# Kernel tuning notes

Hardware: AMD Instinct MI355X
Metric: run time of the kernel (lower is better)

The kernel has to match this reference:

```python
import jax, jax.numpy as jnp
import numpy as np

DIM = 2048
HEADS = 16
B = 2
T = 2048


def setup_inputs() -> dict:
    key = jax.random.key(0)
    k_x, k_qkv, k_out, k_b = jax.random.split(key, 4)
    inv = DIM ** -0.5
    return {
        "x": jax.random.normal(k_x, (B, T, DIM), dtype=jnp.float32),
        "w_qkv": jax.random.normal(k_qkv, (DIM, 3 * DIM), dtype=jnp.float32) * inv,
        "w_out": jax.random.normal(k_out, (DIM, DIM), dtype=jnp.float32) * inv,
        "b_out": jnp.zeros((DIM,), dtype=jnp.float32),
    }


def reference(x, w_qkv, w_out, b_out):
    b, t, e = x.shape
    h = HEADS
    d = e // h
    scale = d ** -0.5
    qkv = x @ w_qkv                              # [b, t, 3e]
    q, k, v = jnp.split(qkv, 3, axis=-1)
    # [b, t, e] -> [b, h, t, d]
    q, k, v = (a.reshape(b, t, h, d).transpose(0, 2, 1, 3) for a in (q, k, v))
    dots = jnp.einsum("bhid,bhjd->bhij", q, k) * scale  # [b, h, t, t]
    causal_mask = jnp.triu(jnp.ones((t, t), dtype=bool), k=1)  # True where j > i
    dots = jnp.where(causal_mask[None, None, :, :], -jnp.inf, dots)
    attn = jax.nn.softmax(dots, axis=-1)
    out = jnp.einsum("bhij,bhjd->bhid", attn, v)  # [b, h, t, d]
    out = out.transpose(0, 2, 1, 3).reshape(b, t, e)
    return out @ w_out + b_out
```

## Files before the change

### kernel.cpp

```cpp
#include <hip/hip_runtime.h>
#include <stdint.h>

#define BATCH 2
#define TDIM 2048
#define EDIM 2048
#define NH 16
#define HD 128
#define E3 6144
#define MROWS 4096

typedef short v8bf __attribute__((ext_vector_type(8)));
typedef float v4f  __attribute__((ext_vector_type(4)));

typedef __attribute__((address_space(3))) uint8_t lds_u8;
typedef __attribute__((address_space(1))) uint8_t glb_u8;

__device__ __forceinline__ void gload16(const void* g, void* l) {
    __builtin_amdgcn_global_load_lds((const glb_u8*)g, (lds_u8*)l, 16, 0, 0);
}

__device__ __forceinline__ ushort f2bf(float f) {
    uint32_t u = __float_as_uint(f);
    return (ushort)((u + 0x7fffu + ((u >> 16) & 1u)) >> 16);
}

__global__ void cvtx_kernel(const float* __restrict__ in, ushort* __restrict__ out, int n) {
    int i = (blockIdx.x * 256 + threadIdx.x) * 4;
    const int stride = gridDim.x * 256 * 4;
    for (; i < n; i += stride) {
        const float4 v = *reinterpret_cast<const float4*>(in + i);
        ushort4 o = make_ushort4(f2bf(v.x), f2bf(v.y), f2bf(v.z), f2bf(v.w));
        *reinterpret_cast<ushort4*>(out + i) = o;
    }
}

__global__ void tcvt_kernel(const float* __restrict__ in, ushort* __restrict__ out, int R, int C) {
    __shared__ float t[32][33];
    const int tc = blockIdx.x * 32;
    const int tr = blockIdx.y * 32;
    const int tid = threadIdx.x;
    const int row = tid >> 3, c4 = (tid & 7) * 4;
    const float4 v = *reinterpret_cast<const float4*>(in + (size_t)(tr + row) * C + tc + c4);
    t[row][c4] = v.x; t[row][c4 + 1] = v.y; t[row][c4 + 2] = v.z; t[row][c4 + 3] = v.w;
    __syncthreads();
    const int oc = tid >> 3, r4 = (tid & 7) * 4;
    ushort4 o = make_ushort4(f2bf(t[r4][oc]), f2bf(t[r4 + 1][oc]),
                             f2bf(t[r4 + 2][oc]), f2bf(t[r4 + 3][oc]));
    *reinterpret_cast<ushort4*>(out + (size_t)(tc + oc) * R + tr + r4) = o;
}

__global__ void vtrans_kernel(const ushort* __restrict__ qkv, ushort* __restrict__ vt) {
    __shared__ ushort t[32][33];
    const int bh = blockIdx.z;
    const int b = bh >> 4, h = bh & 15;
    const int tr = blockIdx.x * 32;
    const int tc = blockIdx.y * 32;
    const int tid = threadIdx.x;
    const int row = tid >> 3, c4 = (tid & 7) * 4;
    const ushort4 v = *reinterpret_cast<const ushort4*>(
        qkv + (size_t)(b * TDIM + tr + row) * E3 + 2 * EDIM + h * HD + tc + c4);
    t[row][c4] = v.x; t[row][c4 + 1] = v.y; t[row][c4 + 2] = v.z; t[row][c4 + 3] = v.w;
    __syncthreads();
    const int oc = tid >> 3, r4 = (tid & 7) * 4;
    ushort4 o = make_ushort4(t[r4][oc], t[r4 + 1][oc], t[r4 + 2][oc], t[r4 + 3][oc]);
    *reinterpret_cast<ushort4*>(vt + (size_t)(bh * HD + tc + oc) * TDIM + tr + r4) = o;
}

template <int OUTF32>
__global__ void gemm_kernel(const ushort* __restrict__ A, const ushort* __restrict__ Bt,
                            void* __restrict__ Cv, const float* __restrict__ bias,
                            int Mdim, int Ndim, int Kdim) {
    __shared__ __align__(16) ushort As[128 * 64];
    __shared__ __align__(16) ushort Bs[128 * 64];
    const int tid = threadIdx.x;
    const int lane = tid & 63;
    const int wv = tid >> 6;
    const int l4 = lane >> 4, l16 = lane & 15;
    const int nbn = Ndim >> 7;
    const int nwg = (Mdim >> 7) * nbn;
    int bid = blockIdx.x;
    bid = (bid & 7) * (nwg >> 3) + (bid >> 3);
    const int bm = bid / nbn, bn = bid % nbn;
    const int wr = wv >> 1, wc = wv & 1;

    const ushort* Abase = A + (size_t)(bm * 128) * Kdim;
    const ushort* Bbase = Bt + (size_t)(bn * 128) * Kdim;

    v4f acc[4][4] = {};

    for (int k0 = 0; k0 < Kdim; k0 += 64) {
#pragma unroll
        for (int i = 0; i < 4; ++i) {
            const int c = i * 256 + tid;
            const int row = c >> 3;
            const int kc = (c & 7) ^ (row & 7);
            gload16(Abase + (size_t)row * Kdim + k0 + kc * 8, &As[(i * 256 + wv * 64) * 8]);
        }
#pragma unroll
        for (int i = 0; i < 4; ++i) {
            const int c = i * 256 + tid;
            const int row = c >> 3;
            const int kc = (c & 7) ^ (row & 7);
            gload16(Bbase + (size_t)row * Kdim + k0 + kc * 8, &Bs[(i * 256 + wv * 64) * 8]);
        }
        __syncthreads();
#pragma unroll
        for (int kk = 0; kk < 2; ++kk) {
            v8bf af[4], bfr[4];
#pragma unroll
            for (int m = 0; m < 4; ++m) {
                const int r = wr * 64 + m * 16 + l16;
                const int slot = (kk * 4 + l4) ^ (r & 7);
                af[m] = *reinterpret_cast<const v8bf*>(&As[r * 64 + slot * 8]);
            }
#pragma unroll
            for (int n = 0; n < 4; ++n) {
                const int r = wc * 64 + n * 16 + l16;
                const int slot = (kk * 4 + l4) ^ (r & 7);
                bfr[n] = *reinterpret_cast<const v8bf*>(&Bs[r * 64 + slot * 8]);
            }
#pragma unroll
            for (int m = 0; m < 4; ++m)
#pragma unroll
                for (int n = 0; n < 4; ++n)
                    acc[m][n] = __builtin_amdgcn_mfma_f32_16x16x32_bf16(af[m], bfr[n], acc[m][n], 0, 0, 0);
        }
        __syncthreads();
    }

    const int r0 = bm * 128 + wr * 64 + l4 * 4;
    const int c0 = bn * 128 + wc * 64 + l16;
    if (OUTF32) {
        float* C = (float*)Cv;
#pragma unroll
        for (int n = 0; n < 4; ++n) {
            const float bv = bias[c0 + n * 16];
#pragma unroll
            for (int m = 0; m < 4; ++m)
#pragma unroll
                for (int j = 0; j < 4; ++j)
                    C[(size_t)(r0 + m * 16 + j) * Ndim + c0 + n * 16] = acc[m][n][j] + bv;
        }
    } else {
        ushort* C = (ushort*)Cv;
#pragma unroll
        for (int n = 0; n < 4; ++n)
#pragma unroll
            for (int m = 0; m < 4; ++m)
#pragma unroll
                for (int j = 0; j < 4; ++j)
                    C[(size_t)(r0 + m * 16 + j) * Ndim + c0 + n * 16] = f2bf(acc[m][n][j]);
    }
}

__global__ __launch_bounds__(256, 2) void flash_kernel(const ushort* __restrict__ qkv,
                                                       const ushort* __restrict__ vt,
                                                       ushort* __restrict__ ao) {
    __shared__ __align__(16) ushort Kl[2][64 * 128];
    __shared__ __align__(16) ushort Vl[2][128 * 64];
    __shared__ __align__(16) ushort Pl[128 * 64];

    const int xi = blockIdx.x;
    const int ti = (xi & 1) ? (xi >> 1) : (15 - (xi >> 1));
    const int h = blockIdx.y;
    const int b = blockIdx.z;
    const int tid = threadIdx.x;
    const int lane = tid & 63;
    const int wv = tid >> 6;
    const int l4 = lane >> 4, l16 = lane & 15;

    const int rbs[2]  = {ti * 64 + wv * 16, TDIM - 64 * (ti + 1) + wv * 16};
    const int diag[2] = {ti, 31 - ti};
    const int nkt = 32 - ti;

    v8bf qf[2][4];
#pragma unroll
    for (int mg = 0; mg < 2; ++mg) {
        const ushort* qp = qkv + (size_t)(b * TDIM + rbs[mg] + l16) * E3 + h * HD + l4 * 8;
#pragma unroll
        for (int d0 = 0; d0 < 4; ++d0) {
            v8bf r = *reinterpret_cast<const v8bf*>(qp + d0 * 32);
            v8bf o;
#pragma unroll
            for (int e = 0; e < 8; ++e) {
                const float f = __uint_as_float(((uint32_t)(ushort)r[e]) << 16) * 0.08838834764831845f;
                o[e] = (short)f2bf(f);
            }
            qf[mg][d0] = o;
        }
    }

    float mrun[2][4], lrun[2][4];
#pragma unroll
    for (int mg = 0; mg < 2; ++mg)
#pragma unroll
        for (int j = 0; j < 4; ++j) { mrun[mg][j] = -1e30f; lrun[mg][j] = 0.0f; }
    v4f oacc[2][8] = {};

    const ushort* kbase = qkv + (size_t)(b * TDIM) * E3 + EDIM + h * HD;
    const ushort* vbase = vt + (size_t)((b * 16 + h) * HD) * TDIM;

#define STAGE(BUF, KT)                                                                        \
    do {                                                                                      \
        _Pragma("unroll") for (int i = 0; i < 4; ++i) {                                       \
            const int c = i * 256 + tid;                                                      \
            const int row = c >> 4;                                                           \
            const int dc = (c & 15) ^ (row & 7);                                              \
            gload16(kbase + (size_t)((KT) * 64 + row) * E3 + dc * 8,                          \
                    &Kl[BUF][(i * 256 + wv * 64) * 8]);                                       \
        }                                                                                     \
        _Pragma("unroll") for (int i = 0; i < 4; ++i) {                                       \
            const int c = i * 256 + tid;                                                      \
            const int row = c >> 3;                                                           \
            const int jc = (c & 7) ^ (row & 7);                                               \
            gload16(vbase + (size_t)row * TDIM + (KT) * 64 + jc * 8,                          \
                    &Vl[BUF][(i * 256 + wv * 64) * 8]);                                       \
        }                                                                                     \
    } while (0)

    STAGE(0, 0);
    __syncthreads();
    int cur = 0;

    for (int kt = 0; kt < nkt; ++kt) {
        if (kt + 1 < nkt) STAGE(cur ^ 1, kt + 1);

        const bool act0 = (kt <= diag[0]);
        const ushort* Kb = &Kl[cur][0];
        const ushort* Vb = &Vl[cur][0];

        v4f s[2][4] = {};
#pragma unroll
        for (int d0 = 0; d0 < 4; ++d0) {
            v8bf kf[4];
#pragma unroll
            for (int kvn = 0; kvn < 4; ++kvn) {
                const int r = kvn * 16 + l16;
                const int slot = (d0 * 4 + l4) ^ (r & 7);
                kf[kvn] = *reinterpret_cast<const v8bf*>(&Kb[r * 128 + slot * 8]);
            }
#pragma unroll
            for (int kvn = 0; kvn < 4; ++kvn) {
                if (act0)
                    s[0][kvn] = __builtin_amdgcn_mfma_f32_16x16x32_bf16(qf[0][d0], kf[kvn], s[0][kvn], 0, 0, 0);
                s[1][kvn] = __builtin_amdgcn_mfma_f32_16x16x32_bf16(qf[1][d0], kf[kvn], s[1][kvn], 0, 0, 0);
            }
        }

#pragma unroll
        for (int mg = 0; mg < 2; ++mg) {
            if (mg == 0 && !act0) continue;

            float sv[4][4];
#pragma unroll
            for (int kvn = 0; kvn < 4; ++kvn)
#pragma unroll
                for (int j = 0; j < 4; ++j)
                    sv[kvn][j] = s[mg][kvn][j];

            if (kt == diag[mg]) {
                const int rg = rbs[mg] + l4 * 4;
#pragma unroll
                for (int kvn = 0; kvn < 4; ++kvn) {
                    const int cg = kt * 64 + kvn * 16 + l16;
#pragma unroll
                    for (int j = 0; j < 4; ++j)
                        if (cg > rg + j) sv[kvn][j] = -__builtin_inff();
                }
            }

            float pm[4], dmax = -1e30f;
#pragma unroll
            for (int j = 0; j < 4; ++j) {
                float m0 = fmaxf(fmaxf(sv[0][j], sv[1][j]), fmaxf(sv[2][j], sv[3][j]));
                m0 = fmaxf(m0, __shfl_xor(m0, 1));
                m0 = fmaxf(m0, __shfl_xor(m0, 2));
                m0 = fmaxf(m0, __shfl_xor(m0, 4));
                m0 = fmaxf(m0, __shfl_xor(m0, 8));
                pm[j] = m0;
                dmax = fmaxf(dmax, m0 - mrun[mg][j]);
            }
            if (!__all(dmax <= 8.0f)) {
                float corr[4];
#pragma unroll
                for (int j = 0; j < 4; ++j) {
                    const float mn = fmaxf(mrun[mg][j], pm[j]);
                    corr[j] = __expf(mrun[mg][j] - mn);
                    mrun[mg][j] = mn;
                    lrun[mg][j] *= corr[j];
                }
#pragma unroll
                for (int n = 0; n < 8; ++n)
#pragma unroll
                    for (int j = 0; j < 4; ++j)
                        oacc[mg][n][j] *= corr[j];
            }

            float p[4][4];
#pragma unroll
            for (int kvn = 0; kvn < 4; ++kvn)
#pragma unroll
                for (int j = 0; j < 4; ++j)
                    p[kvn][j] = __expf(sv[kvn][j] - mrun[mg][j]);
#pragma unroll
            for (int j = 0; j < 4; ++j)
                lrun[mg][j] += p[0][j] + p[1][j] + p[2][j] + p[3][j];

            const int row = wv * 32 + mg * 16 + l4 * 4;
#pragma unroll
            for (int kvn = 0; kvn < 4; ++kvn) {
                const int cc = kvn * 2 + (l16 >> 3);
#pragma unroll
                for (int j = 0; j < 4; ++j) {
                    const int r = row + j;
                    Pl[r * 64 + ((cc ^ (r & 7)) * 8) + (l16 & 7)] = f2bf(p[kvn][j]);
                }
            }
        }

#pragma unroll
        for (int kk = 0; kk < 2; ++kk) {
            v8bf pf[2];
#pragma unroll
            for (int mg = 0; mg < 2; ++mg) {
                if (mg == 0 && !act0) continue;
                const int r = wv * 32 + mg * 16 + l16;
                const int slot = (kk * 4 + l4) ^ (r & 7);
                pf[mg] = *reinterpret_cast<const v8bf*>(&Pl[r * 64 + slot * 8]);
            }
#pragma unroll
            for (int n = 0; n < 8; ++n) {
                const int dr = n * 16 + l16;
                const int slot = (kk * 4 + l4) ^ (dr & 7);
                v8bf vf = *reinterpret_cast<const v8bf*>(&Vb[dr * 64 + slot * 8]);
                if (act0)
                    oacc[0][n] = __builtin_amdgcn_mfma_f32_16x16x32_bf16(pf[0], vf, oacc[0][n], 0, 0, 0);
                oacc[1][n] = __builtin_amdgcn_mfma_f32_16x16x32_bf16(pf[1], vf, oacc[1][n], 0, 0, 0);
            }
        }
        __syncthreads();
        cur ^= 1;
    }
#undef STAGE

#pragma unroll
    for (int mg = 0; mg < 2; ++mg) {
        float inv[4];
#pragma unroll
        for (int j = 0; j < 4; ++j) {
            float l = lrun[mg][j];
            l += __shfl_xor(l, 1);
            l += __shfl_xor(l, 2);
            l += __shfl_xor(l, 4);
            l += __shfl_xor(l, 8);
            inv[j] = 1.0f / l;
        }
        ushort* aop = ao + (size_t)(b * TDIM + rbs[mg] + l4 * 4) * EDIM + h * HD + l16;
#pragma unroll
        for (int n = 0; n < 8; ++n)
#pragma unroll
            for (int j = 0; j < 4; ++j)
                aop[(size_t)j * EDIM + n * 16] = f2bf(oacc[mg][n][j] * inv[j]);
    }
}

extern "C" void kernel_launch(void* const* d_in, const int* in_sizes, int n_in,
                              void* d_out, int out_size, void* d_ws, size_t ws_size,
                              hipStream_t stream) {
    (void)in_sizes; (void)n_in; (void)out_size; (void)ws_size;
    const float* x     = (const float*)d_in[0];
    const float* w_qkv = (const float*)d_in[1];
    const float* w_out = (const float*)d_in[2];
    const float* b_out = (const float*)d_in[3];

    uint8_t* ws = (uint8_t*)d_ws;
    ushort* qkv   = (ushort*)(ws);
    ushort* woutT = (ushort*)(ws + 50331648u);
    ushort* xb    = (ushort*)(ws + 58720256u);
    ushort* wqkvT = (ushort*)(ws + 75497472u);
    ushort* vtb   = xb;
    ushort* ao    = wqkvT;

    cvtx_kernel<<<2048, 256, 0, stream>>>(x, xb, MROWS * EDIM);
    tcvt_kernel<<<dim3(E3 / 32, EDIM / 32), 256, 0, stream>>>(w_qkv, wqkvT, EDIM, E3);
    tcvt_kernel<<<dim3(EDIM / 32, EDIM / 32), 256, 0, stream>>>(w_out, woutT, EDIM, EDIM);

    gemm_kernel<0><<<(MROWS / 128) * (E3 / 128), 256, 0, stream>>>(
        xb, wqkvT, (void*)qkv, nullptr, MROWS, E3, EDIM);

    vtrans_kernel<<<dim3(TDIM / 32, HD / 32, BATCH * NH), 256, 0, stream>>>(qkv, vtb);

    flash_kernel<<<dim3(16, NH, BATCH), 256, 0, stream>>>(qkv, vtb, ao);

    gemm_kernel<1><<<(MROWS / 128) * (EDIM / 128), 256, 0, stream>>>(
        ao, woutT, d_out, b_out, MROWS, EDIM, EDIM);
}
```

Before: 265.1 us.

## Add 256x256 double-buffered QKV GEMM kernel with 8 waves

Replaces the 128x128 QKV projection GEMM with a new 256x256-tile kernel using 512 threads, double-buffered LDS staging via global_load_lds, and a two-stage prefetch pipeline with explicit waitcnt and barriers. Larger tiles raise arithmetic intensity and cut global and L2 traffic, and the prefetch overlaps loads with MFMA work. The kernel uses 128 KB of LDS and many accumulator registers per thread, which limits occupancy, and the grid shrinks to 384 workgroups, which may balance poorly across CUs. Local variable renames in the old GEMM are cosmetic.

```diff
diff --git a/kernel.cpp b/kernel.cpp
--- a/kernel.cpp
+++ b/kernel.cpp
@@ -64,6 +64,120 @@
     const int oc = tid >> 3, r4 = (tid & 7) * 4;
     ushort4 o = make_ushort4(t[r4][oc], t[r4 + 1][oc], t[r4 + 2][oc], t[r4 + 3][oc]);
     *reinterpret_cast<ushort4*>(vt + (size_t)(bh * HD + tc + oc) * TDIM + tr + r4) = o;
+}
+
+__global__ __launch_bounds__(512, 2) void gemm256_kernel(const ushort* __restrict__ A,
+                                                         const ushort* __restrict__ Bt,
+                                                         ushort* __restrict__ C,
+                                                         int Mdim, int Ndim, int Kdim) {
+    __shared__ __align__(16) ushort Al[2][256 * 64];
+    __shared__ __align__(16) ushort Bl[2][256 * 64];
+    const int tid = threadIdx.x;
+    const int lane = tid & 63;
+    const int wv = tid >> 6;
+    const int l4 = lane >> 4, l16 = lane & 15;
+    const int wr = wv >> 2, wc = wv & 3;
+    const int nbn = Ndim >> 8;
+    const int nwg = (Mdim >> 8) * nbn;
+    int bid = blockIdx.x;
+    bid = (bid & 7) * (nwg >> 3) + (bid >> 3);
+    const int bm = bid / nbn, bn = bid % nbn;
+
+    const ushort* Abase = A + (size_t)(bm * 256) * Kdim;
+    const ushort* Bbase = Bt + (size_t)(bn * 256) * Kdim;
+    const int NT = Kdim >> 6;
+
+    v4f acc[8][4] = {};
+
+#define STAGE256(BUF, KT)                                                                     \
+    do {                                                                                      \
+        _Pragma("unroll") for (int i = 0; i < 4; ++i) {                                       \
+            const int c = i * 512 + tid;                                                      \
+            const int row = c >> 3;                                                           \
+            const int kc = (c & 7) ^ (row & 7);                                               \
+            gload16(Abase + (size_t)row * Kdim + (KT) * 64 + kc * 8,                          \
+                    &Al[BUF][(i * 512 + wv * 64) * 8]);                                       \
+        }                                                                                     \
+        _Pragma("unroll") for (int i = 0; i < 4; ++i) {                                       \
+            const int c = i * 512 + tid;                                                      \
+            const int row = c >> 3;                                                           \
+            const int kc = (c & 7) ^ (row & 7);                                               \
+            gload16(Bbase + (size_t)row * Kdim + (KT) * 64 + kc * 8,                          \
+                    &Bl[BUF][(i * 512 + wv * 64) * 8]);                                       \
+        }                                                                                     \
+    } while (0)
+
+    STAGE256(0, 0);
+    STAGE256(1, 1);
+    asm volatile("s_waitcnt vmcnt(8)" ::: "memory");
+    __builtin_amdgcn_s_barrier();
+    asm volatile("" ::: "memory");
+
+    int cur = 0;
+    for (int t = 0; t < NT; ++t) {
+        const ushort* As = &Al[cur][0];
+        const ushort* Bs = &Bl[cur][0];
+#pragma unroll
+        for (int mh = 0; mh < 2; ++mh) {
+            v8bf af[4][2];
+#pragma unroll
+            for (int m = 0; m < 4; ++m)
+#pragma unroll
+                for (int kk = 0; kk < 2; ++kk) {
+                    const int r = wr * 128 + mh * 64 + m * 16 + l16;
+                    const int slot = (kk * 4 + l4) ^ (l16 & 7);
+                    af[m][kk] = *reinterpret_cast<const v8bf*>(&As[r * 64 + slot * 8]);
+                }
+#pragma unroll
+            for (int nh = 0; nh < 2; ++nh) {
+                v8bf bfr[2][2];
+#pragma unroll
+                for (int n = 0; n < 2; ++n)
+#pragma unroll
+                    for (int kk = 0; kk < 2; ++kk) {
+                        const int r = wc * 64 + nh * 32 + n * 16 + l16;
+                        const int slot = (kk * 4 + l4) ^ (l16 & 7);
+                        bfr[n][kk] = *reinterpret_cast<const v8bf*>(&Bs[r * 64 + slot * 8]);
+                    }
+                __builtin_amdgcn_s_setprio(1);
+#pragma unroll
+                for (int kk = 0; kk < 2; ++kk)
+#pragma unroll
+                    for (int m = 0; m < 4; ++m)
+#pragma unroll
+                        for (int n = 0; n < 2; ++n)
+                            acc[mh * 4 + m][nh * 2 + n] = __builtin_amdgcn_mfma_f32_16x16x32_bf16(
+                                af[m][kk], bfr[n][kk], acc[mh * 4 + m][nh * 2 + n], 0, 0, 0);
+                __builtin_amdgcn_s_setprio(0);
+            }
+        }
+        if (t == NT - 1) break;
+
+        __builtin_amdgcn_sched_barrier(0);
+        __builtin_amdgcn_s_barrier();
+        asm volatile("" ::: "memory");
+        if (t + 2 < NT) {
+            STAGE256(cur, t + 2);
+            asm volatile("s_waitcnt vmcnt(8)" ::: "memory");
+        } else {
+            asm volatile("s_waitcnt vmcnt(0)" ::: "memory");
+        }
+        __builtin_amdgcn_s_barrier();
+        asm volatile("" ::: "memory");
+        __builtin_amdgcn_sched_barrier(0);
+        cur ^= 1;
+    }
+#undef STAGE256
+
+    const int r0 = bm * 256 + wr * 128 + l4 * 4;
+    const int c0 = bn * 256 + wc * 64 + l16;
+#pragma unroll
+    for (int mi = 0; mi < 8; ++mi)
+#pragma unroll
+        for (int ni = 0; ni < 4; ++ni)
+#pragma unroll
+            for (int j = 0; j < 4; ++j)
+                C[(size_t)(r0 + mi * 16 + j) * Ndim + c0 + ni * 16] = f2bf(acc[mi][ni][j]);
 }
 
 template <int OUTF32>
@@ -131,7 +245,7 @@
     const int r0 = bm * 128 + wr * 64 + l4 * 4;
     const int c0 = bn * 128 + wc * 64 + l16;
     if (OUTF32) {
-        float* C = (float*)Cv;
+        float* Cf = (float*)Cv;
 #pragma unroll
         for (int n = 0; n < 4; ++n) {
             const float bv = bias[c0 + n * 16];
@@ -139,17 +253,17 @@
             for (int m = 0; m < 4; ++m)
 #pragma unroll
                 for (int j = 0; j < 4; ++j)
-                    C[(size_t)(r0 + m * 16 + j) * Ndim + c0 + n * 16] = acc[m][n][j] + bv;
+                    Cf[(size_t)(r0 + m * 16 + j) * Ndim + c0 + n * 16] = acc[m][n][j] + bv;
         }
     } else {
-        ushort* C = (ushort*)Cv;
+        ushort* Cb = (ushort*)Cv;
 #pragma unroll
         for (int n = 0; n < 4; ++n)
 #pragma unroll
             for (int m = 0; m < 4; ++m)
 #pragma unroll
                 for (int j = 0; j < 4; ++j)
-                    C[(size_t)(r0 + m * 16 + j) * Ndim + c0 + n * 16] = f2bf(acc[m][n][j]);
+                    Cb[(size_t)(r0 + m * 16 + j) * Ndim + c0 + n * 16] = f2bf(acc[m][n][j]);
     }
 }
 
@@ -385,8 +499,8 @@
     tcvt_kernel<<<dim3(E3 / 32, EDIM / 32), 256, 0, stream>>>(w_qkv, wqkvT, EDIM, E3);
     tcvt_kernel<<<dim3(EDIM / 32, EDIM / 32), 256, 0, stream>>>(w_out, woutT, EDIM, EDIM);
 
-    gemm_kernel<0><<<(MROWS / 128) * (E3 / 128), 256, 0, stream>>>(
-        xb, wqkvT, (void*)qkv, nullptr, MROWS, E3, EDIM);
+    gemm256_kernel<<<(MROWS / 256) * (E3 / 256), 512, 0, stream>>>(
+        xb, wqkvT, qkv, MROWS, E3, EDIM);
 
     vtrans_kernel<<<dim3(TDIM / 32, HD / 32, BATCH * NH), 256, 0, stream>>>(qkv, vtb);
 
```

Measured after the change: 289.0 us. +9.0%, slower.

## Rewrite GEMMs as double-buffered 128x256 tiles with split-phase prefetch

Applied to the files above, without the earlier changes.

Replaces the single-buffered 128x128 GEMM with a 512-thread kernel that computes a 128x256 output tile. A and B tiles are double-buffered in LDS, and global loads are split into two chunks issued between the two half-N MFMA phases, using explicit vmcnt waits, barriers and setprio. The goal is to overlap global-to-LDS traffic with MFMA work and to raise the arithmetic intensity of each tile. In exchange, LDS use grows to 96KB per block and the hand-tuned waitcnt counts are fragile, so any miscount could read stale data.

```diff
diff --git a/kernel.cpp b/kernel.cpp
--- a/kernel.cpp
+++ b/kernel.cpp
@@ -67,90 +67,155 @@
 }
 
 template <int OUTF32>
-__global__ void gemm_kernel(const ushort* __restrict__ A, const ushort* __restrict__ Bt,
-                            void* __restrict__ Cv, const float* __restrict__ bias,
-                            int Mdim, int Ndim, int Kdim) {
-    __shared__ __align__(16) ushort As[128 * 64];
-    __shared__ __align__(16) ushort Bs[128 * 64];
+__global__ __launch_bounds__(512, 2) void gemm2p_kernel(const ushort* __restrict__ A,
+                                                        const ushort* __restrict__ Bt,
+                                                        void* __restrict__ Cv,
+                                                        const float* __restrict__ bias,
+                                                        int Mdim, int Ndim, int Kdim) {
+    __shared__ __align__(16) ushort AL[2][128 * 64];
+    __shared__ __align__(16) ushort BL[2][256 * 64];
     const int tid = threadIdx.x;
     const int lane = tid & 63;
     const int wv = tid >> 6;
     const int l4 = lane >> 4, l16 = lane & 15;
-    const int nbn = Ndim >> 7;
+    const int wr = wv >> 2, wc = wv & 3;
+    const int nbn = Ndim >> 8;
     const int nwg = (Mdim >> 7) * nbn;
     int bid = blockIdx.x;
     bid = (bid & 7) * (nwg >> 3) + (bid >> 3);
     const int bm = bid / nbn, bn = bid % nbn;
-    const int wr = wv >> 1, wc = wv & 1;
 
     const ushort* Abase = A + (size_t)(bm * 128) * Kdim;
-    const ushort* Bbase = Bt + (size_t)(bn * 128) * Kdim;
-
-    v4f acc[4][4] = {};
-
-    for (int k0 = 0; k0 < Kdim; k0 += 64) {
-#pragma unroll
-        for (int i = 0; i < 4; ++i) {
-            const int c = i * 256 + tid;
-            const int row = c >> 3;
-            const int kc = (c & 7) ^ (row & 7);
-            gload16(Abase + (size_t)row * Kdim + k0 + kc * 8, &As[(i * 256 + wv * 64) * 8]);
-        }
-#pragma unroll
-        for (int i = 0; i < 4; ++i) {
-            const int c = i * 256 + tid;
-            const int row = c >> 3;
-            const int kc = (c & 7) ^ (row & 7);
-            gload16(Bbase + (size_t)row * Kdim + k0 + kc * 8, &Bs[(i * 256 + wv * 64) * 8]);
-        }
-        __syncthreads();
-#pragma unroll
-        for (int kk = 0; kk < 2; ++kk) {
-            v8bf af[4], bfr[4];
-#pragma unroll
-            for (int m = 0; m < 4; ++m) {
+    const ushort* Bbase = Bt + (size_t)(bn * 256) * Kdim;
+    const int NT = Kdim >> 6;
+
+    const int arow = tid >> 3;
+    const int akc = (tid & 7) ^ (arow & 7);
+
+#define CHUNK0(BUF, T)                                                                       \
+    do {                                                                                     \
+        gload16(Abase + (size_t)arow * Kdim + (T) * 64 + akc * 8,                            \
+                &AL[BUF][(wv * 64) * 8]);                                                    \
+        gload16(Abase + (size_t)(64 + arow) * Kdim + (T) * 64 + akc * 8,                     \
+                &AL[BUF][(512 + wv * 64) * 8]);                                              \
+        gload16(Bbase + (size_t)arow * Kdim + (T) * 64 + akc * 8,                            \
+                &BL[BUF][(wv * 64) * 8]);                                                    \
+        gload16(Bbase + (size_t)(64 + arow) * Kdim + (T) * 64 + akc * 8,                     \
+                &BL[BUF][(512 + wv * 64) * 8]);                                              \
+    } while (0)
+#define CHUNK1(BUF, T)                                                                       \
+    do {                                                                                     \
+        gload16(Bbase + (size_t)(128 + arow) * Kdim + (T) * 64 + akc * 8,                    \
+                &BL[BUF][(1024 + wv * 64) * 8]);                                             \
+        gload16(Bbase + (size_t)(192 + arow) * Kdim + (T) * 64 + akc * 8,                    \
+                &BL[BUF][(1536 + wv * 64) * 8]);                                             \
+    } while (0)
+
+    CHUNK0(0, 0);
+    CHUNK1(0, 0);
+    CHUNK0(1, 1);
+    asm volatile("s_waitcnt vmcnt(4)" ::: "memory");
+    __builtin_amdgcn_s_barrier();
+    __builtin_amdgcn_sched_barrier(0);
+
+    v4f acc[2][4][2] = {};
+
+    for (int t = 0; t < NT; ++t) {
+        const int cur = t & 1;
+        const ushort* As = &AL[cur][0];
+        const ushort* Bs = &BL[cur][0];
+        v8bf af[4][2], bfr[2][2];
+
+#pragma unroll
+        for (int m = 0; m < 4; ++m)
+#pragma unroll
+            for (int kk = 0; kk < 2; ++kk) {
                 const int r = wr * 64 + m * 16 + l16;
-                const int slot = (kk * 4 + l4) ^ (r & 7);
-                af[m] = *reinterpret_cast<const v8bf*>(&As[r * 64 + slot * 8]);
-            }
-#pragma unroll
-            for (int n = 0; n < 4; ++n) {
-                const int r = wc * 64 + n * 16 + l16;
-                const int slot = (kk * 4 + l4) ^ (r & 7);
-                bfr[n] = *reinterpret_cast<const v8bf*>(&Bs[r * 64 + slot * 8]);
-            }
+                const int slot = (kk * 4 + l4) ^ (l16 & 7);
+                af[m][kk] = *reinterpret_cast<const v8bf*>(&As[r * 64 + slot * 8]);
+            }
+#pragma unroll
+        for (int n = 0; n < 2; ++n)
+#pragma unroll
+            for (int kk = 0; kk < 2; ++kk) {
+                const int r = wc * 32 + n * 16 + l16;
+                const int slot = (kk * 4 + l4) ^ (l16 & 7);
+                bfr[n][kk] = *reinterpret_cast<const v8bf*>(&Bs[r * 64 + slot * 8]);
+            }
+        if (t + 1 < NT) CHUNK1(cur ^ 1, t + 1);
+        __builtin_amdgcn_s_barrier();
+        asm volatile("s_waitcnt lgkmcnt(0)" ::: "memory");
+        __builtin_amdgcn_sched_barrier(0);
+        __builtin_amdgcn_s_setprio(1);
+#pragma unroll
+        for (int kk = 0; kk < 2; ++kk)
 #pragma unroll
             for (int m = 0; m < 4; ++m)
 #pragma unroll
-                for (int n = 0; n < 4; ++n)
-                    acc[m][n] = __builtin_amdgcn_mfma_f32_16x16x32_bf16(af[m], bfr[n], acc[m][n], 0, 0, 0);
-        }
-        __syncthreads();
+                for (int n = 0; n < 2; ++n)
+                    acc[0][m][n] = __builtin_amdgcn_mfma_f32_16x16x32_bf16(
+                        af[m][kk], bfr[n][kk], acc[0][m][n], 0, 0, 0);
+        __builtin_amdgcn_s_setprio(0);
+        if (t + 1 < NT)
+            asm volatile("s_waitcnt vmcnt(6)" ::: "memory");
+        else
+            asm volatile("s_waitcnt vmcnt(0)" ::: "memory");
+        __builtin_amdgcn_s_barrier();
+        __builtin_amdgcn_sched_barrier(0);
+
+#pragma unroll
+        for (int n = 0; n < 2; ++n)
+#pragma unroll
+            for (int kk = 0; kk < 2; ++kk) {
+                const int r = 128 + wc * 32 + n * 16 + l16;
+                const int slot = (kk * 4 + l4) ^ (l16 & 7);
+                bfr[n][kk] = *reinterpret_cast<const v8bf*>(&Bs[r * 64 + slot * 8]);
+            }
+        if (t + 2 < NT) CHUNK0(cur, t + 2);
+        __builtin_amdgcn_s_barrier();
+        asm volatile("s_waitcnt lgkmcnt(0)" ::: "memory");
+        __builtin_amdgcn_sched_barrier(0);
+        __builtin_amdgcn_s_setprio(1);
+#pragma unroll
+        for (int kk = 0; kk < 2; ++kk)
+#pragma unroll
+            for (int m = 0; m < 4; ++m)
+#pragma unroll
+                for (int n = 0; n < 2; ++n)
+                    acc[1][m][n] = __builtin_amdgcn_mfma_f32_16x16x32_bf16(
+                        af[m][kk], bfr[n][kk], acc[1][m][n], 0, 0, 0);
+        __builtin_amdgcn_s_setprio(0);
+        if (t + 2 < NT)
+            asm volatile("s_waitcnt vmcnt(6)" ::: "memory");
+        else if (t + 1 < NT)
+            asm volatile("s_waitcnt vmcnt(2)" ::: "memory");
+        __builtin_amdgcn_s_barrier();
+        __builtin_amdgcn_sched_barrier(0);
     }
-
-    const int r0 = bm * 128 + wr * 64 + l4 * 4;
-    const int c0 = bn * 128 + wc * 64 + l16;
-    if (OUTF32) {
-        float* C = (float*)Cv;
-#pragma unroll
-        for (int n = 0; n < 4; ++n) {
-            const float bv = bias[c0 + n * 16];
-#pragma unroll
-            for (int m = 0; m < 4; ++m)
-#pragma unroll
-                for (int j = 0; j < 4; ++j)
-                    C[(size_t)(r0 + m * 16 + j) * Ndim + c0 + n * 16] = acc[m][n][j] + bv;
-        }
-    } else {
-        ushort* C = (ushort*)Cv;
-#pragma unroll
-        for (int n = 0; n < 4; ++n)
-#pragma unroll
-            for (int m = 0; m < 4; ++m)
-#pragma unroll
-                for (int j = 0; j < 4; ++j)
-                    C[(size_t)(r0 + m * 16 + j) * Ndim + c0 + n * 16] = f2bf(acc[m][n][j]);
-    }
+#undef CHUNK0
+#undef CHUNK1
+
+#pragma unroll
+    for (int nh = 0; nh < 2; ++nh)
+#pragma unroll
+        for (int m = 0; m < 4; ++m)
+#pragma unroll
+            for (int n = 0; n < 2; ++n) {
+                const int r0 = bm * 128 + wr * 64 + m * 16 + l4 * 4;
+                const int c0 = bn * 256 + nh * 128 + wc * 32 + n * 16 + l16;
+                if (OUTF32) {
+                    float* Cf = (float*)Cv;
+                    const float bv = bias[c0];
+#pragma unroll
+                    for (int j = 0; j < 4; ++j)
+                        Cf[(size_t)(r0 + j) * Ndim + c0] = acc[nh][m][n][j] + bv;
+                } else {
+                    ushort* Cb = (ushort*)Cv;
+#pragma unroll
+                    for (int j = 0; j < 4; ++j)
+                        Cb[(size_t)(r0 + j) * Ndim + c0] = f2bf(acc[nh][m][n][j]);
+                }
+            }
 }
 
 __global__ __launch_bounds__(256, 2) void flash_kernel(const ushort* __restrict__ qkv,
@@ -385,13 +450,13 @@
     tcvt_kernel<<<dim3(E3 / 32, EDIM / 32), 256, 0, stream>>>(w_qkv, wqkvT, EDIM, E3);
     tcvt_kernel<<<dim3(EDIM / 32, EDIM / 32), 256, 0, stream>>>(w_out, woutT, EDIM, EDIM);
 
-    gemm_kernel<0><<<(MROWS / 128) * (E3 / 128), 256, 0, stream>>>(
+    gemm2p_kernel<0><<<(MROWS / 128) * (E3 / 256), 512, 0, stream>>>(
         xb, wqkvT, (void*)qkv, nullptr, MROWS, E3, EDIM);
 
     vtrans_kernel<<<dim3(TDIM / 32, HD / 32, BATCH * NH), 256, 0, stream>>>(qkv, vtb);
 
     flash_kernel<<<dim3(16, NH, BATCH), 256, 0, stream>>>(qkv, vtb, ao);
 
-    gemm_kernel<1><<<(MROWS / 128) * (EDIM / 128), 256, 0, stream>>>(
+    gemm2p_kernel<1><<<(MROWS / 128) * (EDIM / 256), 512, 0, stream>>>(
         ao, woutT, d_out, b_out, MROWS, EDIM, EDIM);
 }
```

After: 275.0 us. 1.04x slower.

## Fuse V transpose into QKV GEMM epilogue and merge prep kernels

Applied to the files above, without the earlier changes.

The QKV GEMM now writes Q and K into a narrower buffer and writes V directly in transposed per-head layout from its epilogue, which removes the separate vtrans kernel and its read/write pass. The three input conversion kernels are merged into a single prep launch to save launch overhead. In exchange, the V epilogue stores 4 contiguous bf16 values per lane at TDIM stride, which is less coalesced than the normal row-major stores. The workspace layout is also changed so that V^T no longer aliases xb.

```diff
diff --git a/kernel.cpp b/kernel.cpp
--- a/kernel.cpp
+++ b/kernel.cpp
@@ -8,6 +8,7 @@
 #define HD 128
 #define E3 6144
 #define MROWS 4096
+#define QKS 4096
 
 typedef short v8bf __attribute__((ext_vector_type(8)));
 typedef float v4f  __attribute__((ext_vector_type(4)));
@@ -24,21 +25,10 @@
     return (ushort)((u + 0x7fffu + ((u >> 16) & 1u)) >> 16);
 }
 
-__global__ void cvtx_kernel(const float* __restrict__ in, ushort* __restrict__ out, int n) {
-    int i = (blockIdx.x * 256 + threadIdx.x) * 4;
-    const int stride = gridDim.x * 256 * 4;
-    for (; i < n; i += stride) {
-        const float4 v = *reinterpret_cast<const float4*>(in + i);
-        ushort4 o = make_ushort4(f2bf(v.x), f2bf(v.y), f2bf(v.z), f2bf(v.w));
-        *reinterpret_cast<ushort4*>(out + i) = o;
-    }
-}
-
-__global__ void tcvt_kernel(const float* __restrict__ in, ushort* __restrict__ out, int R, int C) {
+__device__ __forceinline__ void tcvt_body(const float* __restrict__ in, ushort* __restrict__ out,
+                                          int R, int C, int tcb, int trb, int tid) {
     __shared__ float t[32][33];
-    const int tc = blockIdx.x * 32;
-    const int tr = blockIdx.y * 32;
-    const int tid = threadIdx.x;
+    const int tc = tcb * 32, tr = trb * 32;
     const int row = tid >> 3, c4 = (tid & 7) * 4;
     const float4 v = *reinterpret_cast<const float4*>(in + (size_t)(tr + row) * C + tc + c4);
     t[row][c4] = v.x; t[row][c4 + 1] = v.y; t[row][c4 + 2] = v.z; t[row][c4 + 3] = v.w;
@@ -49,26 +39,37 @@
     *reinterpret_cast<ushort4*>(out + (size_t)(tc + oc) * R + tr + r4) = o;
 }
 
-__global__ void vtrans_kernel(const ushort* __restrict__ qkv, ushort* __restrict__ vt) {
-    __shared__ ushort t[32][33];
-    const int bh = blockIdx.z;
-    const int b = bh >> 4, h = bh & 15;
-    const int tr = blockIdx.x * 32;
-    const int tc = blockIdx.y * 32;
+#define NB_T1 12288
+#define NB_T2 4096
+#define NB_CV 2048
+
+__global__ void prep_kernel(const float* __restrict__ x, const float* __restrict__ w_qkv,
+                            const float* __restrict__ w_out, ushort* __restrict__ xb,
+                            ushort* __restrict__ wqkvT, ushort* __restrict__ woutT) {
+    const int bid = blockIdx.x;
     const int tid = threadIdx.x;
-    const int row = tid >> 3, c4 = (tid & 7) * 4;
-    const ushort4 v = *reinterpret_cast<const ushort4*>(
-        qkv + (size_t)(b * TDIM + tr + row) * E3 + 2 * EDIM + h * HD + tc + c4);
-    t[row][c4] = v.x; t[row][c4 + 1] = v.y; t[row][c4 + 2] = v.z; t[row][c4 + 3] = v.w;
-    __syncthreads();
-    const int oc = tid >> 3, r4 = (tid & 7) * 4;
-    ushort4 o = make_ushort4(t[r4][oc], t[r4 + 1][oc], t[r4 + 2][oc], t[r4 + 3][oc]);
-    *reinterpret_cast<ushort4*>(vt + (size_t)(bh * HD + tc + oc) * TDIM + tr + r4) = o;
-}
-
-template <int OUTF32>
+    if (bid < NB_T1) {
+        tcvt_body(w_qkv, wqkvT, EDIM, E3, bid % (E3 / 32), bid / (E3 / 32), tid);
+    } else if (bid < NB_T1 + NB_T2) {
+        const int b2 = bid - NB_T1;
+        tcvt_body(w_out, woutT, EDIM, EDIM, b2 % (EDIM / 32), b2 / (EDIM / 32), tid);
+    } else {
+        const int b3 = bid - NB_T1 - NB_T2;
+        int i = (b3 * 256 + tid) * 4;
+        const int stride = NB_CV * 256 * 4;
+        const int n = MROWS * EDIM;
+        for (; i < n; i += stride) {
+            const float4 v = *reinterpret_cast<const float4*>(x + i);
+            ushort4 o = make_ushort4(f2bf(v.x), f2bf(v.y), f2bf(v.z), f2bf(v.w));
+            *reinterpret_cast<ushort4*>(xb + i) = o;
+        }
+    }
+}
+
+template <int MODE>
 __global__ void gemm_kernel(const ushort* __restrict__ A, const ushort* __restrict__ Bt,
                             void* __restrict__ Cv, const float* __restrict__ bias,
+                            ushort* __restrict__ vtout,
                             int Mdim, int Ndim, int Kdim) {
     __shared__ __align__(16) ushort As[128 * 64];
     __shared__ __align__(16) ushort Bs[128 * 64];
@@ -130,8 +131,8 @@
 
     const int r0 = bm * 128 + wr * 64 + l4 * 4;
     const int c0 = bn * 128 + wc * 64 + l16;
-    if (OUTF32) {
-        float* C = (float*)Cv;
+    if (MODE == 1) {
+        float* Cf = (float*)Cv;
 #pragma unroll
         for (int n = 0; n < 4; ++n) {
             const float bv = bias[c0 + n * 16];
@@ -139,21 +140,37 @@
             for (int m = 0; m < 4; ++m)
 #pragma unroll
                 for (int j = 0; j < 4; ++j)
-                    C[(size_t)(r0 + m * 16 + j) * Ndim + c0 + n * 16] = acc[m][n][j] + bv;
+                    Cf[(size_t)(r0 + m * 16 + j) * Ndim + c0 + n * 16] = acc[m][n][j] + bv;
+        }
+    } else if (MODE == 2 && bn >= 32) {
+        const int h = bn - 32;
+#pragma unroll
+        for (int m = 0; m < 4; ++m) {
+            const int r = r0 + m * 16;
+            const int b = r >> 11, t0 = r & 2047;
+#pragma unroll
+            for (int n = 0; n < 4; ++n) {
+                const int dcol = wc * 64 + n * 16 + l16;
+                ushort* vp = vtout + (size_t)((b * 16 + h) * 128 + dcol) * TDIM + t0;
+#pragma unroll
+                for (int j = 0; j < 4; ++j)
+                    vp[j] = f2bf(acc[m][n][j]);
+            }
         }
     } else {
-        ushort* C = (ushort*)Cv;
+        const int cstride = (MODE == 2) ? QKS : Ndim;
+        ushort* Cb = (ushort*)Cv;
 #pragma unroll
         for (int n = 0; n < 4; ++n)
 #pragma unroll
             for (int m = 0; m < 4; ++m)
 #pragma unroll
                 for (int j = 0; j < 4; ++j)
-                    C[(size_t)(r0 + m * 16 + j) * Ndim + c0 + n * 16] = f2bf(acc[m][n][j]);
-    }
-}
-
-__global__ __launch_bounds__(256, 2) void flash_kernel(const ushort* __restrict__ qkv,
+                    Cb[(size_t)(r0 + m * 16 + j) * cstride + c0 + n * 16] = f2bf(acc[m][n][j]);
+    }
+}
+
+__global__ __launch_bounds__(256, 2) void flash_kernel(const ushort* __restrict__ qk,
                                                        const ushort* __restrict__ vt,
                                                        ushort* __restrict__ ao) {
     __shared__ __align__(16) ushort Kl[2][64 * 128];
@@ -176,7 +193,7 @@
     v8bf qf[2][4];
 #pragma unroll
     for (int mg = 0; mg < 2; ++mg) {
-        const ushort* qp = qkv + (size_t)(b * TDIM + rbs[mg] + l16) * E3 + h * HD + l4 * 8;
+        const ushort* qp = qk + (size_t)(b * TDIM + rbs[mg] + l16) * QKS + h * HD + l4 * 8;
 #pragma unroll
         for (int d0 = 0; d0 < 4; ++d0) {
             v8bf r = *reinterpret_cast<const v8bf*>(qp + d0 * 32);
@@ -197,7 +214,7 @@
         for (int j = 0; j < 4; ++j) { mrun[mg][j] = -1e30f; lrun[mg][j] = 0.0f; }
     v4f oacc[2][8] = {};
 
-    const ushort* kbase = qkv + (size_t)(b * TDIM) * E3 + EDIM + h * HD;
+    const ushort* kbase = qk + (size_t)(b * TDIM) * QKS + EDIM + h * HD;
     const ushort* vbase = vt + (size_t)((b * 16 + h) * HD) * TDIM;
 
 #define STAGE(BUF, KT)                                                                        \
@@ -206,7 +223,7 @@
             const int c = i * 256 + tid;                                                      \
             const int row = c >> 4;                                                           \
             const int dc = (c & 15) ^ (row & 7);                                              \
-            gload16(kbase + (size_t)((KT) * 64 + row) * E3 + dc * 8,                          \
+            gload16(kbase + (size_t)((KT) * 64 + row) * QKS + dc * 8,                         \
                     &Kl[BUF][(i * 256 + wv * 64) * 8]);                                       \
         }                                                                                     \
         _Pragma("unroll") for (int i = 0; i < 4; ++i) {                                       \
@@ -374,24 +391,20 @@
     const float* b_out = (const float*)d_in[3];
 
     uint8_t* ws = (uint8_t*)d_ws;
-    ushort* qkv   = (ushort*)(ws);
+    ushort* qk    = (ushort*)(ws);
+    ushort* vtb   = (ushort*)(ws + 33554432u);
     ushort* woutT = (ushort*)(ws + 50331648u);
     ushort* xb    = (ushort*)(ws + 58720256u);
     ushort* wqkvT = (ushort*)(ws + 75497472u);
-    ushort* vtb   = xb;
     ushort* ao    = wqkvT;
 
-    cvtx_kernel<<<2048, 256, 0, stream>>>(x, xb, MROWS * EDIM);
-    tcvt_kernel<<<dim3(E3 / 32, EDIM / 32), 256, 0, stream>>>(w_qkv, wqkvT, EDIM, E3);
-    tcvt_kernel<<<dim3(EDIM / 32, EDIM / 32), 256, 0, stream>>>(w_out, woutT, EDIM, EDIM);
-
-    gemm_kernel<0><<<(MROWS / 128) * (E3 / 128), 256, 0, stream>>>(
-        xb, wqkvT, (void*)qkv, nullptr, MROWS, E3, EDIM);
-
-    vtrans_kernel<<<dim3(TDIM / 32, HD / 32, BATCH * NH), 256, 0, stream>>>(qkv, vtb);
-
-    flash_kernel<<<dim3(16, NH, BATCH), 256, 0, stream>>>(qkv, vtb, ao);
+    prep_kernel<<<NB_T1 + NB_T2 + NB_CV, 256, 0, stream>>>(x, w_qkv, w_out, xb, wqkvT, woutT);
+
+    gemm_kernel<2><<<(MROWS / 128) * (E3 / 128), 256, 0, stream>>>(
+        xb, wqkvT, (void*)qk, nullptr, vtb, MROWS, E3, EDIM);
+
+    flash_kernel<<<dim3(16, NH, BATCH), 256, 0, stream>>>(qk, vtb, ao);
 
     gemm_kernel<1><<<(MROWS / 128) * (EDIM / 128), 256, 0, stream>>>(
-        ao, woutT, d_out, b_out, MROWS, EDIM, EDIM);
-}
+        ao, woutT, d_out, b_out, nullptr, MROWS, EDIM, EDIM);
+}
```

New measurement: 256.4 us. 3.3% less time.
